# Performance work log

Hardware: AMD Instinct MI355X
Metric: run time of the kernel (lower is better)

## Reference

```python
import jax, jax.numpy as jnp
import numpy as np

N, P, C_IN, C_OUT, C_FEAT = 100000, 32, 4, 64, 9
BN_EPS = 1e-3


def setup_inputs() -> dict:
    key = jax.random.key(0)
    k1, k2, k3, k4 = jax.random.split(key, 4)
    voxels = jax.random.normal(k1, (N, P, C_IN), dtype=jnp.float32)
    num_points_per_voxel = jax.random.randint(k2, (N,), 1, P + 1, dtype=jnp.int32)
    voxel_centers = jax.random.normal(k3, (N, 2), dtype=jnp.float32)
    W = jax.random.normal(k4, (C_OUT, C_FEAT), dtype=jnp.float32) * (1.0 / np.sqrt(C_FEAT))
    gamma = jnp.ones((C_OUT,), dtype=jnp.float32)
    beta = jnp.zeros((C_OUT,), dtype=jnp.float32)
    return {"voxels": voxels, "num_points_per_voxel": num_points_per_voxel,
            "voxel_centers": voxel_centers, "W": W, "gamma": gamma, "beta": beta}


def reference(voxels, num_points_per_voxel, voxel_centers, W, gamma, beta):
    npts = num_points_per_voxel.astype(voxels.dtype)[:, None, None]  # [N,1,1]
    # cluster offset: per-pillar mean of xyz
    points_mean = voxels[:, :, :3].sum(axis=1, keepdims=True) / npts  # [N,1,3]
    f_cluster = voxels[:, :, :3] - points_mean                        # [N,P,3]
    # center offset: xy minus Cartesian voxel center
    f_center = voxels[:, :, :2] - voxel_centers[:, None, :]           # [N,P,2]
    features = jnp.concatenate([voxels, f_cluster, f_center], axis=-1)  # [N,P,9]
    # zero out padded points
    mask = num_points_per_voxel[:, None] > jnp.arange(P, dtype=jnp.int32)[None, :]
    features = features * mask[:, :, None].astype(features.dtype)
    # PFNLayer (last_layer=True): linear(no bias) -> BN(batch stats) -> relu -> max over points
    x = jnp.einsum('npc,oc->npo', features, W)  # [N,P,64]
    mean = x.mean(axis=(0, 1))
    var = ((x - mean) ** 2).mean(axis=(0, 1))   # biased var, as torch BN training
    x = (x - mean) * jax.lax.rsqrt(var + BN_EPS) * gamma + beta
    x = jax.nn.relu(x)
    return x.max(axis=1)  # [N,64]
```

## Files before the change

kernel.cpp:

```cpp
#include <hip/hip_runtime.h>
#include <math.h>

#define N_PILLARS 100000
#define N_PAIRS   (N_PILLARS / 2)
#define P_PTS 32
#define BN_EPS 1e-3f

typedef short v8s __attribute__((ext_vector_type(8)));
typedef float v16f __attribute__((ext_vector_type(16)));

__device__ __forceinline__ unsigned short f2bf(float f) {
    unsigned int u = __float_as_uint(f);
    return (unsigned short)((u + 0x8000u) >> 16);
}


__global__ __launch_bounds__(256, 4) void pfn_stats(
    const float* __restrict__ vox,
    const int*   __restrict__ npts,
    const float* __restrict__ ctr,
    float*       __restrict__ gstats,
    float4*      __restrict__ means)
{
    __shared__ float smem[4][54];
    const int tid = threadIdx.x, wave = tid >> 6, lane = tid & 63;
    const int pl = lane & 31, half = lane >> 5;

    float F[9], M[45];
#pragma unroll
    for (int j = 0; j < 9; ++j) F[j] = 0.f;
#pragma unroll
    for (int j = 0; j < 45; ++j) M[j] = 0.f;

    const int wid = blockIdx.x * 4 + wave, nw = gridDim.x * 4;
    for (int pr = wid; pr < N_PAIRS; pr += nw) {
        const int n0 = pr * 2;
        const float4 pt = ((const float4*)(vox + (size_t)n0 * 128))[lane];
        const int2   np2 = ((const int2*)npts)[pr];
        const float4 c4  = ((const float4*)ctr)[pr];
        const int   np  = half ? np2.y : np2.x;
        const float cx  = half ? c4.z : c4.x;
        const float cy  = half ? c4.w : c4.y;

        float sx = pt.x, sy = pt.y, sz = pt.z;
#pragma unroll
        for (int m = 1; m <= 16; m <<= 1) {
            sx += __shfl_xor(sx, m); sy += __shfl_xor(sy, m); sz += __shfl_xor(sz, m);
        }
        const float inv = 1.f / (float)np;
        const float mx = sx * inv, my = sy * inv, mz = sz * inv;
        if (pl == 0)
            means[n0 + half] = make_float4(mx, my, mz, (float)np);

        const bool valid = pl < np;
        float f[9];
        f[0] = valid ? pt.x : 0.f;
        f[1] = valid ? pt.y : 0.f;
        f[2] = valid ? pt.z : 0.f;
        f[3] = valid ? pt.w : 0.f;
        f[4] = valid ? (pt.x - mx) : 0.f;
        f[5] = valid ? (pt.y - my) : 0.f;
        f[6] = valid ? (pt.z - mz) : 0.f;
        f[7] = valid ? (pt.x - cx) : 0.f;
        f[8] = valid ? (pt.y - cy) : 0.f;

#pragma unroll
        for (int j = 0; j < 9; ++j) F[j] += f[j];
        int idx = 0;
#pragma unroll
        for (int k = 0; k < 9; ++k)
#pragma unroll
            for (int j = k; j < 9; ++j) { M[idx] = fmaf(f[k], f[j], M[idx]); ++idx; }
    }

#pragma unroll
    for (int j = 0; j < 9; ++j)
#pragma unroll
        for (int m = 1; m < 64; m <<= 1) F[j] += __shfl_xor(F[j], m);
#pragma unroll
    for (int j = 0; j < 45; ++j)
#pragma unroll
        for (int m = 1; m < 64; m <<= 1) M[j] += __shfl_xor(M[j], m);

    if (lane == 0) {
#pragma unroll
        for (int j = 0; j < 9; ++j)  smem[wave][j]     = F[j];
#pragma unroll
        for (int j = 0; j < 45; ++j) smem[wave][9 + j] = M[j];
    }
    __syncthreads();
    if (tid < 54) {
        const float v = smem[0][tid] + smem[1][tid] + smem[2][tid] + smem[3][tid];
        atomicAdd(&gstats[tid], v);
    }
}

__global__ __launch_bounds__(256, 4) void pfn_max(
    const float*  __restrict__ vox,
    const int*    __restrict__ npts,
    const float*  __restrict__ ctr,
    const float*  __restrict__ W,
    const float*  __restrict__ gstats,
    const float*  __restrict__ gamma,
    const float*  __restrict__ beta,
    const float4* __restrict__ means,
    float*        __restrict__ out)
{
    const int tid = threadIdx.x, wave = tid >> 6, lane = tid & 63;
    const int col = lane & 31;
    const bool blo = (lane < 32);
    const int ch = lane;

    float Wr[9];
#pragma unroll
    for (int j = 0; j < 9; ++j) Wr[j] = W[ch * 9 + j];

    const float invNP = 1.f / (float)(N_PILLARS * P_PTS);
    float mean = 0.f;
#pragma unroll
    for (int j = 0; j < 9; ++j) mean = fmaf(Wr[j], gstats[j], mean);
    mean *= invNP;
    float q = 0.f;
    {
        int idx = 0;
#pragma unroll
        for (int k = 0; k < 9; ++k)
#pragma unroll
            for (int j = k; j < 9; ++j) {
                const float coef = (j == k) ? 1.f : 2.f;
                q = fmaf(coef * Wr[k] * Wr[j], gstats[9 + idx], q);
                ++idx;
            }
    }
    const float var = q * invNP - mean * mean;
    const float sc  = gamma[ch] * rsqrtf(var + BN_EPS);
    const float bs  = beta[ch] - mean * sc;

    v8s Bm0 = {0,0,0,0,0,0,0,0}, Bm1 = Bm0;
    if (blo) {
        const int c0 = col, c1 = 32 + col;
        Bm0[0] = (short)f2bf(W[c0*9+0] + W[c0*9+4] + W[c0*9+7]);
        Bm0[1] = (short)f2bf(W[c0*9+1] + W[c0*9+5] + W[c0*9+8]);
        Bm0[2] = (short)f2bf(W[c0*9+2] + W[c0*9+6]);
        Bm0[3] = (short)f2bf(W[c0*9+3]);
        Bm0[4] = (short)f2bf(-1e30f);
        Bm1[0] = (short)f2bf(W[c1*9+0] + W[c1*9+4] + W[c1*9+7]);
        Bm1[1] = (short)f2bf(W[c1*9+1] + W[c1*9+5] + W[c1*9+8]);
        Bm1[2] = (short)f2bf(W[c1*9+2] + W[c1*9+6]);
        Bm1[3] = (short)f2bf(W[c1*9+3]);
        Bm1[4] = (short)f2bf(-1e30f);
    }

    v16f z;
#pragma unroll
    for (int r = 0; r < 16; ++r) z[r] = 0.f;

    const int wid = blockIdx.x * 4 + wave, nw = gridDim.x * 4;
    for (int n = wid; n < N_PILLARS; n += nw) {
        const int np = npts[n];
        float4 pt = make_float4(0.f, 0.f, 0.f, 0.f);
        if (blo) pt = ((const float4*)(vox + (size_t)n * 128))[col];
        const float4 m = means[n];
        const float2 c = ((const float2*)ctr)[n];

        v8s A = {0,0,0,0,0,0,0,0};
        A[0] = (short)f2bf(pt.x); A[1] = (short)f2bf(pt.y);
        A[2] = (short)f2bf(pt.z); A[3] = (short)f2bf(pt.w);
        A[4] = (blo && col >= np) ? (short)0x3F80 : (short)0;

        const v16f Dm0 = __builtin_amdgcn_mfma_f32_32x32x16_bf16(A, Bm0, z, 0, 0, 0);
        const v16f Dm1 = __builtin_amdgcn_mfma_f32_32x32x16_bf16(A, Bm1, z, 0, 0, 0);

        const float t = -(m.x*Wr[4] + m.y*Wr[5] + m.z*Wr[6] + c.x*Wr[7] + c.y*Wr[8]);

        float h0 = Dm0[0], h1 = Dm1[0];
#pragma unroll
        for (int r = 1; r < 16; ++r) {
            h0 = fmaxf(h0, Dm0[r]);
            h1 = fmaxf(h1, Dm1[r]);
        }
        h0 = fmaxf(h0, __shfl_xor(h0, 32));
        h1 = fmaxf(h1, __shfl_xor(h1, 32));

        float H = (blo ? h0 : h1) + t;
        if (np < P_PTS) H = fmaxf(H, 0.f);

        out[(size_t)n * 64 + ch] = fmaxf(0.f, fmaf(H, sc, bs));
    }
}

extern "C" void kernel_launch(void* const* d_in, const int* in_sizes, int n_in,
                              void* d_out, int out_size, void* d_ws, size_t ws_size,
                              hipStream_t stream) {
    const float* voxels  = (const float*)d_in[0];
    const int*   npts    = (const int*)d_in[1];
    const float* centers = (const float*)d_in[2];
    const float* W       = (const float*)d_in[3];
    const float* gamma   = (const float*)d_in[4];
    const float* beta    = (const float*)d_in[5];
    float* out = (float*)d_out;

    float*  gstats = (float*)d_ws;
    float4* means  = (float4*)((char*)d_ws + 1024);

    hipMemsetAsync(d_ws, 0, 256, stream);
    pfn_stats<<<2048, 256, 0, stream>>>(voxels, npts, centers, gstats, means);
    pfn_max<<<2048, 256, 0, stream>>>(voxels, npts, centers, W, gstats, gamma, beta, means, out);
}
```

Baseline: 173.9 us.

## Fuse stats and pre-BN max into one pass, apply BN in a finish kernel

Merges the statistics pass and the MFMA max pass into a single kernel that reads each voxel pair once, with triple-buffered prefetching and DPP-based reductions. It writes the pre-normalization max to the output, and a second elementwise kernel applies the BN scale/bias and ReLU. This removes the second read of the voxel tensor and the means buffer, but adds a read-modify-write pass over the output. Fixed chunking per wave may cause load imbalance.

```diff
diff --git a/kernel.cpp b/kernel.cpp
--- a/kernel.cpp
+++ b/kernel.cpp
@@ -2,139 +2,63 @@
 #include <math.h>
 
 #define N_PILLARS 100000
-#define N_PAIRS   (N_PILLARS / 2)
-#define P_PTS 32
-#define BN_EPS 1e-3f
-
-typedef short v8s __attribute__((ext_vector_type(8)));
+#define N_PAIRS   50000
+#define P_PTS     32
+#define BN_EPS    1e-3f
+#define ABLOCKS   1024
+#define AWAVES    (ABLOCKS * 4)
+#define CHUNK     13
+
+typedef short v8s  __attribute__((ext_vector_type(8)));
 typedef float v16f __attribute__((ext_vector_type(16)));
 
 __device__ __forceinline__ unsigned short f2bf(float f) {
-    unsigned int u = __float_as_uint(f);
+    unsigned u = __float_as_uint(f);
     return (unsigned short)((u + 0x8000u) >> 16);
 }
-
-
-__global__ __launch_bounds__(256, 4) void pfn_stats(
+#define DPP_ADD(v, ctrl, rmask)                                              \
+    (v) += __int_as_float(__builtin_amdgcn_update_dpp(                       \
+        0, __float_as_int(v), (ctrl), (rmask), 0xF, true))
+__device__ __forceinline__ float halfsum(float v) {
+    DPP_ADD(v, 0x111, 0xF);
+    DPP_ADD(v, 0x112, 0xF);
+    DPP_ADD(v, 0x114, 0xF);
+    DPP_ADD(v, 0x118, 0xF);
+    DPP_ADD(v, 0x142, 0xA);
+    return v;
+}
+__device__ __forceinline__ float fullsum(float v) {
+    v = halfsum(v);
+    DPP_ADD(v, 0x143, 0xC);
+    return v;
+}
+__device__ __forceinline__ float rdlane(float v, int l) {
+    return __int_as_float(__builtin_amdgcn_readlane(__float_as_int(v), l));
+}
+__device__ __forceinline__ float max16(v16f d) {
+    float m = d[0];
+#pragma unroll
+    for (int r = 1; r < 16; ++r) m = fmaxf(m, d[r]);
+    return m;
+}
+
+
+__global__ __launch_bounds__(256, 3) void pfn_pass1(
     const float* __restrict__ vox,
     const int*   __restrict__ npts,
     const float* __restrict__ ctr,
+    const float* __restrict__ W,
     float*       __restrict__ gstats,
-    float4*      __restrict__ means)
+    float*       __restrict__ out)
 {
     __shared__ float smem[4][54];
     const int tid = threadIdx.x, wave = tid >> 6, lane = tid & 63;
-    const int pl = lane & 31, half = lane >> 5;
-
-    float F[9], M[45];
-#pragma unroll
-    for (int j = 0; j < 9; ++j) F[j] = 0.f;
-#pragma unroll
-    for (int j = 0; j < 45; ++j) M[j] = 0.f;
-
-    const int wid = blockIdx.x * 4 + wave, nw = gridDim.x * 4;
-    for (int pr = wid; pr < N_PAIRS; pr += nw) {
-        const int n0 = pr * 2;
-        const float4 pt = ((const float4*)(vox + (size_t)n0 * 128))[lane];
-        const int2   np2 = ((const int2*)npts)[pr];
-        const float4 c4  = ((const float4*)ctr)[pr];
-        const int   np  = half ? np2.y : np2.x;
-        const float cx  = half ? c4.z : c4.x;
-        const float cy  = half ? c4.w : c4.y;
-
-        float sx = pt.x, sy = pt.y, sz = pt.z;
-#pragma unroll
-        for (int m = 1; m <= 16; m <<= 1) {
-            sx += __shfl_xor(sx, m); sy += __shfl_xor(sy, m); sz += __shfl_xor(sz, m);
-        }
-        const float inv = 1.f / (float)np;
-        const float mx = sx * inv, my = sy * inv, mz = sz * inv;
-        if (pl == 0)
-            means[n0 + half] = make_float4(mx, my, mz, (float)np);
-
-        const bool valid = pl < np;
-        float f[9];
-        f[0] = valid ? pt.x : 0.f;
-        f[1] = valid ? pt.y : 0.f;
-        f[2] = valid ? pt.z : 0.f;
-        f[3] = valid ? pt.w : 0.f;
-        f[4] = valid ? (pt.x - mx) : 0.f;
-        f[5] = valid ? (pt.y - my) : 0.f;
-        f[6] = valid ? (pt.z - mz) : 0.f;
-        f[7] = valid ? (pt.x - cx) : 0.f;
-        f[8] = valid ? (pt.y - cy) : 0.f;
-
-#pragma unroll
-        for (int j = 0; j < 9; ++j) F[j] += f[j];
-        int idx = 0;
-#pragma unroll
-        for (int k = 0; k < 9; ++k)
-#pragma unroll
-            for (int j = k; j < 9; ++j) { M[idx] = fmaf(f[k], f[j], M[idx]); ++idx; }
-    }
-
-#pragma unroll
-    for (int j = 0; j < 9; ++j)
-#pragma unroll
-        for (int m = 1; m < 64; m <<= 1) F[j] += __shfl_xor(F[j], m);
-#pragma unroll
-    for (int j = 0; j < 45; ++j)
-#pragma unroll
-        for (int m = 1; m < 64; m <<= 1) M[j] += __shfl_xor(M[j], m);
-
-    if (lane == 0) {
-#pragma unroll
-        for (int j = 0; j < 9; ++j)  smem[wave][j]     = F[j];
-#pragma unroll
-        for (int j = 0; j < 45; ++j) smem[wave][9 + j] = M[j];
-    }
-    __syncthreads();
-    if (tid < 54) {
-        const float v = smem[0][tid] + smem[1][tid] + smem[2][tid] + smem[3][tid];
-        atomicAdd(&gstats[tid], v);
-    }
-}
-
-__global__ __launch_bounds__(256, 4) void pfn_max(
-    const float*  __restrict__ vox,
-    const int*    __restrict__ npts,
-    const float*  __restrict__ ctr,
-    const float*  __restrict__ W,
-    const float*  __restrict__ gstats,
-    const float*  __restrict__ gamma,
-    const float*  __restrict__ beta,
-    const float4* __restrict__ means,
-    float*        __restrict__ out)
-{
-    const int tid = threadIdx.x, wave = tid >> 6, lane = tid & 63;
     const int col = lane & 31;
     const bool blo = (lane < 32);
-    const int ch = lane;
-
-    float Wr[9];
-#pragma unroll
-    for (int j = 0; j < 9; ++j) Wr[j] = W[ch * 9 + j];
-
-    const float invNP = 1.f / (float)(N_PILLARS * P_PTS);
-    float mean = 0.f;
-#pragma unroll
-    for (int j = 0; j < 9; ++j) mean = fmaf(Wr[j], gstats[j], mean);
-    mean *= invNP;
-    float q = 0.f;
-    {
-        int idx = 0;
-#pragma unroll
-        for (int k = 0; k < 9; ++k)
-#pragma unroll
-            for (int j = k; j < 9; ++j) {
-                const float coef = (j == k) ? 1.f : 2.f;
-                q = fmaf(coef * Wr[k] * Wr[j], gstats[9 + idx], q);
-                ++idx;
-            }
-    }
-    const float var = q * invNP - mean * mean;
-    const float sc  = gamma[ch] * rsqrtf(var + BN_EPS);
-    const float bs  = beta[ch] - mean * sc;
+
+    float tw[5];
+#pragma unroll
+    for (int j = 0; j < 5; ++j) tw[j] = W[lane * 9 + 4 + j];
 
     v8s Bm0 = {0,0,0,0,0,0,0,0}, Bm1 = Bm0;
     if (blo) {
@@ -151,41 +75,173 @@
         Bm1[4] = (short)f2bf(-1e30f);
     }
 
+    float F[9], M[45];
+#pragma unroll
+    for (int j = 0; j < 9; ++j) F[j] = 0.f;
+#pragma unroll
+    for (int j = 0; j < 45; ++j) M[j] = 0.f;
+
     v16f z;
 #pragma unroll
     for (int r = 0; r < 16; ++r) z[r] = 0.f;
 
-    const int wid = blockIdx.x * 4 + wave, nw = gridDim.x * 4;
-    for (int n = wid; n < N_PILLARS; n += nw) {
-        const int np = npts[n];
-        float4 pt = make_float4(0.f, 0.f, 0.f, 0.f);
-        if (blo) pt = ((const float4*)(vox + (size_t)n * 128))[col];
-        const float4 m = means[n];
-        const float2 c = ((const float2*)ctr)[n];
-
-        v8s A = {0,0,0,0,0,0,0,0};
-        A[0] = (short)f2bf(pt.x); A[1] = (short)f2bf(pt.y);
-        A[2] = (short)f2bf(pt.z); A[3] = (short)f2bf(pt.w);
-        A[4] = (blo && col >= np) ? (short)0x3F80 : (short)0;
-
-        const v16f Dm0 = __builtin_amdgcn_mfma_f32_32x32x16_bf16(A, Bm0, z, 0, 0, 0);
-        const v16f Dm1 = __builtin_amdgcn_mfma_f32_32x32x16_bf16(A, Bm1, z, 0, 0, 0);
-
-        const float t = -(m.x*Wr[4] + m.y*Wr[5] + m.z*Wr[6] + c.x*Wr[7] + c.y*Wr[8]);
-
-        float h0 = Dm0[0], h1 = Dm1[0];
-#pragma unroll
-        for (int r = 1; r < 16; ++r) {
-            h0 = fmaxf(h0, Dm0[r]);
-            h1 = fmaxf(h1, Dm1[r]);
+    const int wid = blockIdx.x * 4 + wave;
+    const int base = wid * CHUNK;
+
+    float4 buf[3];
+    buf[0] = make_float4(0.f, 0.f, 0.f, 0.f);
+    buf[1] = buf[0]; buf[2] = buf[0];
+    if (base < N_PAIRS)     buf[0] = ((const float4*)vox)[(size_t)base * 64 + lane];
+    if (base + 1 < N_PAIRS) buf[1] = ((const float4*)vox)[(size_t)(base + 1) * 64 + lane];
+
+#pragma unroll
+    for (int i = 0; i < CHUNK; ++i) {
+        const int pr = base + i;
+        if (i + 2 < CHUNK && pr + 2 < N_PAIRS)
+            buf[(i + 2) % 3] = ((const float4*)vox)[(size_t)(pr + 2) * 64 + lane];
+        if (pr < N_PAIRS) {
+            const float4 ptc = buf[i % 3];
+            const int2   np2 = ((const int2*)npts)[pr];
+            const float4 c4  = ((const float4*)ctr)[pr];
+            const int np0 = np2.x, np1 = np2.y;
+
+            const float sxr = halfsum(ptc.x);
+            const float syr = halfsum(ptc.y);
+            const float szr = halfsum(ptc.z);
+            const float i0 = 1.f / (float)np0, i1 = 1.f / (float)np1;
+            const float mx0 = rdlane(sxr, 31) * i0, my0 = rdlane(syr, 31) * i0,
+                        mz0 = rdlane(szr, 31) * i0;
+            const float mx1 = rdlane(sxr, 63) * i1, my1 = rdlane(syr, 63) * i1,
+                        mz1 = rdlane(szr, 63) * i1;
+
+            const int   np  = blo ? np0 : np1;
+            const float mxh = blo ? mx0 : mx1;
+            const float myh = blo ? my0 : my1;
+            const float mzh = blo ? mz0 : mz1;
+            const float cxh = blo ? c4.x : c4.z;
+            const float cyh = blo ? c4.y : c4.w;
+            const bool valid = col < np;
+            float f[9];
+            f[0] = valid ? ptc.x : 0.f;
+            f[1] = valid ? ptc.y : 0.f;
+            f[2] = valid ? ptc.z : 0.f;
+            f[3] = valid ? ptc.w : 0.f;
+            f[4] = valid ? (ptc.x - mxh) : 0.f;
+            f[5] = valid ? (ptc.y - myh) : 0.f;
+            f[6] = valid ? (ptc.z - mzh) : 0.f;
+            f[7] = valid ? (ptc.x - cxh) : 0.f;
+            f[8] = valid ? (ptc.y - cyh) : 0.f;
+#pragma unroll
+            for (int j = 0; j < 9; ++j) F[j] += f[j];
+            {
+                int idx = 0;
+#pragma unroll
+                for (int k = 0; k < 9; ++k)
+#pragma unroll
+                    for (int j = k; j < 9; ++j) { M[idx] = fmaf(f[k], f[j], M[idx]); ++idx; }
+            }
+
+            const int r0 = (int)f2bf(ptc.x) | ((int)f2bf(ptc.y) << 16);
+            const int r1 = (int)f2bf(ptc.z) | ((int)f2bf(ptc.w) << 16);
+            const int q0 = __shfl_xor(r0, 32);
+            const int q1 = __shfl_xor(r1, 32);
+            const int fl0 = (col >= np0) ? 0x3F80 : 0;
+            const int fl1 = (col >= np1) ? 0x3F80 : 0;
+            union { int i[4]; v8s v; } ua, ub;
+            ua.i[0] = blo ? r0 : 0;  ua.i[1] = blo ? r1 : 0;
+            ua.i[2] = blo ? fl0 : 0; ua.i[3] = 0;
+            ub.i[0] = blo ? q0 : 0;  ub.i[1] = blo ? q1 : 0;
+            ub.i[2] = blo ? fl1 : 0; ub.i[3] = 0;
+
+            v16f D;
+            D = __builtin_amdgcn_mfma_f32_32x32x16_bf16(ua.v, Bm0, z, 0, 0, 0);
+            float h00 = max16(D);
+            D = __builtin_amdgcn_mfma_f32_32x32x16_bf16(ua.v, Bm1, z, 0, 0, 0);
+            float h01 = max16(D);
+            D = __builtin_amdgcn_mfma_f32_32x32x16_bf16(ub.v, Bm0, z, 0, 0, 0);
+            float h10 = max16(D);
+            D = __builtin_amdgcn_mfma_f32_32x32x16_bf16(ub.v, Bm1, z, 0, 0, 0);
+            float h11 = max16(D);
+            h00 = fmaxf(h00, __shfl_xor(h00, 32));
+            h01 = fmaxf(h01, __shfl_xor(h01, 32));
+            h10 = fmaxf(h10, __shfl_xor(h10, 32));
+            h11 = fmaxf(h11, __shfl_xor(h11, 32));
+
+            const float t0 = -(mx0*tw[0] + my0*tw[1] + mz0*tw[2] + c4.x*tw[3] + c4.y*tw[4]);
+            const float t1 = -(mx1*tw[0] + my1*tw[1] + mz1*tw[2] + c4.z*tw[3] + c4.w*tw[4]);
+            float H0 = (blo ? h00 : h01) + t0;
+            float H1 = (blo ? h10 : h11) + t1;
+            if (np0 < P_PTS) H0 = fmaxf(H0, 0.f);
+            if (np1 < P_PTS) H1 = fmaxf(H1, 0.f);
+            out[(size_t)(2 * pr) * 64 + lane]     = H0;
+            out[(size_t)(2 * pr + 1) * 64 + lane] = H1;
         }
-        h0 = fmaxf(h0, __shfl_xor(h0, 32));
-        h1 = fmaxf(h1, __shfl_xor(h1, 32));
-
-        float H = (blo ? h0 : h1) + t;
-        if (np < P_PTS) H = fmaxf(H, 0.f);
-
-        out[(size_t)n * 64 + ch] = fmaxf(0.f, fmaf(H, sc, bs));
+    }
+
+#pragma unroll
+    for (int j = 0; j < 9; ++j)  F[j] = fullsum(F[j]);
+#pragma unroll
+    for (int j = 0; j < 45; ++j) M[j] = fullsum(M[j]);
+    if (lane == 63) {
+#pragma unroll
+        for (int j = 0; j < 9; ++j)  smem[wave][j]     = F[j];
+#pragma unroll
+        for (int j = 0; j < 45; ++j) smem[wave][9 + j] = M[j];
+    }
+    __syncthreads();
+    if (tid < 54)
+        atomicAdd(&gstats[tid],
+                  smem[0][tid] + smem[1][tid] + smem[2][tid] + smem[3][tid]);
+}
+
+__global__ __launch_bounds__(256) void pfn_finish(
+    const float* __restrict__ gstats,
+    const float* __restrict__ W,
+    const float* __restrict__ gamma,
+    const float* __restrict__ beta,
+    float*       __restrict__ out)
+{
+    __shared__ float s_sc[64], s_bs[64];
+    const int tid = threadIdx.x;
+    if (tid < 64) {
+        float Wr[9];
+#pragma unroll
+        for (int j = 0; j < 9; ++j) Wr[j] = W[tid * 9 + j];
+        const float invNP = 1.f / (float)(N_PILLARS * P_PTS);
+        float mean = 0.f;
+#pragma unroll
+        for (int j = 0; j < 9; ++j) mean = fmaf(Wr[j], gstats[j], mean);
+        mean *= invNP;
+        float q = 0.f;
+        int idx = 0;
+#pragma unroll
+        for (int k = 0; k < 9; ++k)
+#pragma unroll
+            for (int j = k; j < 9; ++j) {
+                const float coef = (j == k) ? 1.f : 2.f;
+                q = fmaf(coef * Wr[k] * Wr[j], gstats[9 + idx], q);
+                ++idx;
+            }
+        const float var = q * invNP - mean * mean;
+        const float sc  = gamma[tid] * rsqrtf(var + BN_EPS);
+        s_sc[tid] = sc;
+        s_bs[tid] = beta[tid] - mean * sc;
+    }
+    __syncthreads();
+
+    const int g = blockIdx.x * 256 + tid;
+    const int ch0 = (g * 4) & 63;
+    const float4 sc4 = *(const float4*)&s_sc[ch0];
+    const float4 bs4 = *(const float4*)&s_bs[ch0];
+    const int total4 = N_PILLARS * 16;
+    const int stride = gridDim.x * 256;
+    for (int i = g; i < total4; i += stride) {
+        float4 v = ((float4*)out)[i];
+        v.x = fmaxf(0.f, fmaf(v.x, sc4.x, bs4.x));
+        v.y = fmaxf(0.f, fmaf(v.y, sc4.y, bs4.y));
+        v.z = fmaxf(0.f, fmaf(v.z, sc4.z, bs4.z));
+        v.w = fmaxf(0.f, fmaf(v.w, sc4.w, bs4.w));
+        ((float4*)out)[i] = v;
     }
 }
 
@@ -198,12 +254,10 @@
     const float* W       = (const float*)d_in[3];
     const float* gamma   = (const float*)d_in[4];
     const float* beta    = (const float*)d_in[5];
-    float* out = (float*)d_out;
-
-    float*  gstats = (float*)d_ws;
-    float4* means  = (float4*)((char*)d_ws + 1024);
+    float* out    = (float*)d_out;
+    float* gstats = (float*)d_ws;
 
     hipMemsetAsync(d_ws, 0, 256, stream);
-    pfn_stats<<<2048, 256, 0, stream>>>(voxels, npts, centers, gstats, means);
-    pfn_max<<<2048, 256, 0, stream>>>(voxels, npts, centers, W, gstats, gamma, beta, means, out);
-}
+    pfn_pass1<<<ABLOCKS, 256, 0, stream>>>(voxels, npts, centers, W, gstats, out);
+    pfn_finish<<<2048, 256, 0, stream>>>(gstats, W, gamma, beta, out);
+}
```

After: 144.4 us. 17.0% less time.
